# Optimization experiments

Measured on AMD Instinct MI355X. Metric: run time of the kernel, lower is better.

## Reference

```python
import jax, jax.numpy as jnp
import numpy as np
import math

N, S, C, K, V = 32, 4096, 1, 512, 128
TARGET_SCALE = 0.06  # normalize_scale == embedding_scale when normalize=True


def setup_inputs() -> dict:
    key = jax.random.key(0)
    k1, k2 = jax.random.split(key)
    x0 = jax.random.normal(k1, (N, S, C, V), dtype=jnp.float32)
    emb = jax.random.normal(k2, (C, K, V), dtype=jnp.float32) * TARGET_SCALE
    # after_update(): renormalize each code vector to norm = embedding_scale*sqrt(V)
    tn = TARGET_SCALE * math.sqrt(V)
    emb = emb * (tn / jnp.linalg.norm(emb, axis=2, keepdims=True))
    return {"x0": x0, "embedding0": emb}


def _vq_forward(x0, embedding0):
    tn = TARGET_SCALE * math.sqrt(V)
    # normalize inputs and codebook to the same norm (normalize=True path)
    x = tn * x0 / jnp.linalg.norm(x0, axis=3, keepdims=True)              # (N,S,C,V)
    emb = tn * embedding0 / jnp.linalg.norm(embedding0, axis=2, keepdims=True)  # (C,K,V)

    xf = x.reshape(N * S, C, V)
    x2 = jnp.sum(xf * xf, axis=2)                     # (NS, C)
    e2 = jnp.sum(emb * emb, axis=2)                   # (C, K)
    dots = jnp.einsum('ncv,ckv->nck', xf, emb)        # (NS, C, K)
    d2 = x2[:, :, None] + e2[None, :, :] - 2.0 * dots
    index = jnp.argmin(d2, axis=2)                    # (NS, C) int

    # entropy of code usage: histc over n_classes, normalized by len(index)=NS
    hist = jnp.zeros((K,), jnp.float32).at[index.reshape(-1)].add(1.0)
    prob = hist / float(N * S)
    entropy = -jnp.sum(jnp.where(hist > 0, prob * jnp.log(jnp.where(hist > 0, prob, 1.0)), 0.0))

    # gather selected code vectors per channel
    output = emb[jnp.arange(C)[None, :], index]       # (NS, C, V)
    output = output.reshape(x.shape)                  # (N,S,C,V)

    sg = jax.lax.stop_gradient
    out0 = sg(output - x) + x                                              # straight-through
    out1 = jnp.sum((sg(x) - output) ** 2, axis=3)                          # codebook loss (N,S,C)
    out2 = jnp.sum((x - sg(output)) ** 2, axis=3) + jnp.sum((x - x0) ** 2, axis=3)  # commitment + norm penalty
    return out0, out1, out2, entropy


def reference(x0, embedding0):
    return _vq_forward(x0, embedding0)
```

## Files before the change

### kernel.cpp

```cpp
#include <hip/hip_runtime.h>
#include <math.h>

#define VDIM   128
#define KCODES 512
#define NROWS  (32 * 4096)
#define TILE_ROWS 128
#define STAGE_CODES 128
#define STAGE_GRAN (STAGE_CODES * 16)
#define TN 0.67882250993908565f

typedef __attribute__((ext_vector_type(8))) short bf16x8;
typedef __attribute__((ext_vector_type(4))) float f32x4;

__device__ __forceinline__ unsigned short f2bf(float f) {
    unsigned u = __float_as_uint(f);
    unsigned r = u + 0x7FFFu + ((u >> 16) & 1u);
    return (unsigned short)(r >> 16);
}

__device__ __forceinline__ bf16x8 pack8(float4 a, float4 b) {
    bf16x8 v;
    v[0] = (short)f2bf(a.x); v[1] = (short)f2bf(a.y);
    v[2] = (short)f2bf(a.z); v[3] = (short)f2bf(a.w);
    v[4] = (short)f2bf(b.x); v[5] = (short)f2bf(b.y);
    v[6] = (short)f2bf(b.z); v[7] = (short)f2bf(b.w);
    return v;
}

__global__ void prep_emb(const float* __restrict__ emb0,
                         float* __restrict__ embn,
                         unsigned short* __restrict__ ebf) {
    int k = blockIdx.x;
    int l = threadIdx.x;
    const float* row = emb0 + (size_t)k * VDIM;
    float a = row[l];
    float b = row[l + 64];
    float ss = a * a + b * b;
    #pragma unroll
    for (int off = 32; off; off >>= 1) ss += __shfl_xor(ss, off);
    float nrm = sqrtf(ss);
    float ea = (TN * a) / nrm;
    float eb = (TN * b) / nrm;
    embn[(size_t)k * VDIM + l]      = ea;
    embn[(size_t)k * VDIM + l + 64] = eb;
    ebf[(size_t)k * VDIM + l]      = f2bf(ea);
    ebf[(size_t)k * VDIM + l + 64] = f2bf(eb);
}

__global__ __launch_bounds__(256, 4) void vq_main(
        const float* __restrict__ x0,
        const unsigned short* __restrict__ ebf,
        const float* __restrict__ embn,
        unsigned* __restrict__ hist,
        float* __restrict__ out0,
        float* __restrict__ out1,
        float* __restrict__ out2) {
    __shared__ uint4 sB[STAGE_GRAN];
    __shared__ int   sbesti[TILE_ROWS];
    __shared__ float sdot[TILE_ROWS];
    __shared__ float sn0[TILE_ROWS];

    int t = threadIdx.x;
    int w = t >> 6;
    int l = t & 63;
    int n15 = l & 15;
    int q = l >> 4;

    int rowbase = blockIdx.x * TILE_ROWS + (w << 5);
    bf16x8 afr[2][4];
    float nsq[2];
    #pragma unroll
    for (int s = 0; s < 2; ++s) {
        const float* xrow = x0 + (size_t)(rowbase + (s << 4) + n15) * VDIM + (q << 3);
        float p0 = 0.f, p1 = 0.f;
        #pragma unroll
        for (int kc = 0; kc < 4; ++kc) {
            const float4* xp = (const float4*)(xrow + (kc << 5));
            float4 a = xp[0], b = xp[1];
            p0 = fmaf(a.x, a.x, p0); p1 = fmaf(a.y, a.y, p1);
            p0 = fmaf(a.z, a.z, p0); p1 = fmaf(a.w, a.w, p1);
            p0 = fmaf(b.x, b.x, p0); p1 = fmaf(b.y, b.y, p1);
            p0 = fmaf(b.z, b.z, p0); p1 = fmaf(b.w, b.w, p1);
            afr[s][kc] = pack8(a, b);
        }
        nsq[s] = p0 + p1;
        nsq[s] += __shfl_xor(nsq[s], 16, 64);
        nsq[s] += __shfl_xor(nsq[s], 32, 64);
    }

    float best[2][4];
    int   bidx[2][4];
    #pragma unroll
    for (int s = 0; s < 2; ++s)
        #pragma unroll
        for (int r = 0; r < 4; ++r) { best[s][r] = -3.4e38f; bidx[s][r] = 0; }

    const f32x4 zero4 = {0.f, 0.f, 0.f, 0.f};
    const uint4* ebg = (const uint4*)ebf;

    for (int st = 0; st < 4; ++st) {
        if (st) __syncthreads();

        #pragma unroll
        for (int r = 0; r < 8; ++r) {
            int code = st * STAGE_CODES + (r << 4) + (t & 15);
            int gran = ((t >> 6) << 2) + ((t >> 4) & 3);
            sB[(r << 8) + t] = ebg[(size_t)code * 16 + gran];
        }
        __syncthreads();

        #pragma unroll 2
        for (int cn8 = 0; cn8 < 8; ++cn8) {
            const bf16x8* bls = ((const bf16x8*)sB) + (cn8 << 8) + l;
            bf16x8 b0 = bls[0], b1 = bls[64], b2 = bls[128], b3 = bls[192];
            int nbase = st * STAGE_CODES + (cn8 << 4) + n15;
            #pragma unroll
            for (int s = 0; s < 2; ++s) {
                f32x4 acc = __builtin_amdgcn_mfma_f32_16x16x32_bf16(afr[s][0], b0, zero4, 0, 0, 0);
                acc = __builtin_amdgcn_mfma_f32_16x16x32_bf16(afr[s][1], b1, acc, 0, 0, 0);
                acc = __builtin_amdgcn_mfma_f32_16x16x32_bf16(afr[s][2], b2, acc, 0, 0, 0);
                acc = __builtin_amdgcn_mfma_f32_16x16x32_bf16(afr[s][3], b3, acc, 0, 0, 0);
                #pragma unroll
                for (int r = 0; r < 4; ++r) {
                    float d = acc[r];
                    if (d > best[s][r]) { best[s][r] = d; bidx[s][r] = nbase; }
                }
            }
        }
    }

    #pragma unroll
    for (int m = 1; m <= 8; m <<= 1) {
        #pragma unroll
        for (int s = 0; s < 2; ++s)
            #pragma unroll
            for (int r = 0; r < 4; ++r) {
                float ov = __shfl_xor(best[s][r], m, 64);
                int   oi = __shfl_xor(bidx[s][r], m, 64);
                if (ov > best[s][r] || (ov == best[s][r] && oi < bidx[s][r])) {
                    best[s][r] = ov; bidx[s][r] = oi;
                }
            }
    }

    if (n15 == 0) {
        #pragma unroll
        for (int s = 0; s < 2; ++s)
            #pragma unroll
            for (int r = 0; r < 4; ++r) {
                int lr = (w << 5) + (s << 4) + (q << 2) + r;
                sbesti[lr] = bidx[s][r];
                sdot[lr]   = best[s][r];
            }
    }
    if (q == 0) {
        #pragma unroll
        for (int s = 0; s < 2; ++s) sn0[(w << 5) + (s << 4) + n15] = nsq[s];
    }
    __syncthreads();

    size_t blockrow = (size_t)blockIdx.x * TILE_ROWS;
    #pragma unroll
    for (int pass = 0; pass < 16; ++pass) {
        int lr = (pass << 3) + (t >> 5);
        int v4 = t & 31;
        int bi = sbesti[lr];
        float4 e = ((const float4*)(embn + (size_t)bi * VDIM))[v4];
        ((float4*)(out0 + (blockrow + lr) * (size_t)VDIM))[v4] = e;
    }

    if (t < TILE_ROWS) {
        size_t row = blockrow + t;
        int bi = sbesti[t];
        float dotv = sdot[t];
        float nn = sn0[t];
        float sc = TN / sqrtf(nn);
        float o1 = 2.f * TN * TN - 2.f * sc * dotv;
        out1[row] = o1;
        float sm = sc - 1.f;
        out2[row] = o1 + sm * sm * nn;
        atomicAdd(&hist[bi], 1u);
    }
}

__global__ void entropy_k(const unsigned* __restrict__ hist,
                          float* __restrict__ out) {
    __shared__ float red[8];
    int t = threadIdx.x;
    float h = (float)hist[t];
    float p = h / (float)NROWS;
    float term = (h > 0.f) ? p * logf(p) : 0.f;
    #pragma unroll
    for (int off = 32; off; off >>= 1) term += __shfl_xor(term, off);
    if ((t & 63) == 0) red[t >> 6] = term;
    __syncthreads();
    if (t == 0) {
        float ssum = 0.f;
        #pragma unroll
        for (int i = 0; i < 8; i++) ssum += red[i];
        out[0] = -ssum;
    }
}

extern "C" void kernel_launch(void* const* d_in, const int* in_sizes, int n_in,
                              void* d_out, int out_size, void* d_ws, size_t ws_size,
                              hipStream_t stream) {
    const float* x0   = (const float*)d_in[0];
    const float* emb0 = (const float*)d_in[1];

    float* embn = (float*)d_ws;
    unsigned* hist = (unsigned*)(embn + (size_t)KCODES * VDIM);
    unsigned short* ebf = (unsigned short*)(hist + KCODES);

    float* out  = (float*)d_out;
    float* out0 = out;
    float* out1 = out0 + (size_t)NROWS * VDIM;
    float* out2 = out1 + NROWS;
    float* oent = out2 + NROWS;

    hipMemsetAsync(hist, 0, KCODES * sizeof(unsigned), stream);
    prep_emb<<<KCODES, 64, 0, stream>>>(emb0, embn, ebf);
    vq_main<<<NROWS / TILE_ROWS, 256, 0, stream>>>(x0, ebf, embn, hist,
                                                   out0, out1, out2);
    entropy_k<<<1, KCODES, 0, stream>>>(hist, oent);
}
```

Before: 166.1 us.

## Halve row tile, fuse entropy into last block, gather output from bf16 codebook

Shrinks the row tile and code stage to 64, raising launch bounds to 8 waves so more blocks can be resident and hide memory latency. The entropy reduction moves into the main kernel using a last-block atomic counter, removing a separate launch. The fp32 normalized codebook buffer is dropped, and out0 is reconstructed from the bf16 codebook. This saves a buffer write, but the output now carries bf16 rounding error, and each block re-stages the full codebook for half as many rows.

```diff
diff --git a/kernel.cpp b/kernel.cpp
--- a/kernel.cpp
+++ b/kernel.cpp
@@ -4,8 +4,9 @@
 #define VDIM   128
 #define KCODES 512
 #define NROWS  (32 * 4096)
-#define TILE_ROWS 128
-#define STAGE_CODES 128
+#define TILE_ROWS 64
+#define NBLOCKS (NROWS / TILE_ROWS)
+#define STAGE_CODES 64
 #define STAGE_GRAN (STAGE_CODES * 16)
 #define TN 0.67882250993908565f
 
@@ -16,6 +17,10 @@
     unsigned u = __float_as_uint(f);
     unsigned r = u + 0x7FFFu + ((u >> 16) & 1u);
     return (unsigned short)(r >> 16);
+}
+
+__device__ __forceinline__ float bf2f(unsigned short h) {
+    return __uint_as_float(((unsigned)h) << 16);
 }
 
 __device__ __forceinline__ bf16x8 pack8(float4 a, float4 b) {
@@ -28,7 +33,6 @@
 }
 
 __global__ void prep_emb(const float* __restrict__ emb0,
-                         float* __restrict__ embn,
                          unsigned short* __restrict__ ebf) {
     int k = blockIdx.x;
     int l = threadIdx.x;
@@ -39,26 +43,25 @@
     #pragma unroll
     for (int off = 32; off; off >>= 1) ss += __shfl_xor(ss, off);
     float nrm = sqrtf(ss);
-    float ea = (TN * a) / nrm;
-    float eb = (TN * b) / nrm;
-    embn[(size_t)k * VDIM + l]      = ea;
-    embn[(size_t)k * VDIM + l + 64] = eb;
-    ebf[(size_t)k * VDIM + l]      = f2bf(ea);
-    ebf[(size_t)k * VDIM + l + 64] = f2bf(eb);
-}
-
-__global__ __launch_bounds__(256, 4) void vq_main(
+    ebf[(size_t)k * VDIM + l]      = f2bf((TN * a) / nrm);
+    ebf[(size_t)k * VDIM + l + 64] = f2bf((TN * b) / nrm);
+}
+
+__global__ __launch_bounds__(256, 8) void vq_main(
         const float* __restrict__ x0,
         const unsigned short* __restrict__ ebf,
-        const float* __restrict__ embn,
         unsigned* __restrict__ hist,
+        unsigned* __restrict__ counter,
         float* __restrict__ out0,
         float* __restrict__ out1,
-        float* __restrict__ out2) {
+        float* __restrict__ out2,
+        float* __restrict__ oent) {
     __shared__ uint4 sB[STAGE_GRAN];
     __shared__ int   sbesti[TILE_ROWS];
     __shared__ float sdot[TILE_ROWS];
     __shared__ float sn0[TILE_ROWS];
+    __shared__ float sred[8];
+    __shared__ int   slast;
 
     int t = threadIdx.x;
     int w = t >> 6;
@@ -66,12 +69,11 @@
     int n15 = l & 15;
     int q = l >> 4;
 
-    int rowbase = blockIdx.x * TILE_ROWS + (w << 5);
-    bf16x8 afr[2][4];
-    float nsq[2];
-    #pragma unroll
-    for (int s = 0; s < 2; ++s) {
-        const float* xrow = x0 + (size_t)(rowbase + (s << 4) + n15) * VDIM + (q << 3);
+    int rowbase = blockIdx.x * TILE_ROWS + (w << 4);
+    bf16x8 afr[4];
+    float nsq;
+    {
+        const float* xrow = x0 + (size_t)(rowbase + n15) * VDIM + (q << 3);
         float p0 = 0.f, p1 = 0.f;
         #pragma unroll
         for (int kc = 0; kc < 4; ++kc) {
@@ -81,91 +83,80 @@
             p0 = fmaf(a.z, a.z, p0); p1 = fmaf(a.w, a.w, p1);
             p0 = fmaf(b.x, b.x, p0); p1 = fmaf(b.y, b.y, p1);
             p0 = fmaf(b.z, b.z, p0); p1 = fmaf(b.w, b.w, p1);
-            afr[s][kc] = pack8(a, b);
-        }
-        nsq[s] = p0 + p1;
-        nsq[s] += __shfl_xor(nsq[s], 16, 64);
-        nsq[s] += __shfl_xor(nsq[s], 32, 64);
-    }
-
-    float best[2][4];
-    int   bidx[2][4];
-    #pragma unroll
-    for (int s = 0; s < 2; ++s)
-        #pragma unroll
-        for (int r = 0; r < 4; ++r) { best[s][r] = -3.4e38f; bidx[s][r] = 0; }
+            afr[kc] = pack8(a, b);
+        }
+        nsq = p0 + p1;
+        nsq += __shfl_xor(nsq, 16, 64);
+        nsq += __shfl_xor(nsq, 32, 64);
+    }
+
+    float best[4];
+    int   bidx[4];
+    #pragma unroll
+    for (int r = 0; r < 4; ++r) { best[r] = -3.4e38f; bidx[r] = 0; }
 
     const f32x4 zero4 = {0.f, 0.f, 0.f, 0.f};
     const uint4* ebg = (const uint4*)ebf;
 
-    for (int st = 0; st < 4; ++st) {
+    for (int st = 0; st < 8; ++st) {
         if (st) __syncthreads();
 
         #pragma unroll
-        for (int r = 0; r < 8; ++r) {
+        for (int r = 0; r < 4; ++r) {
             int code = st * STAGE_CODES + (r << 4) + (t & 15);
             int gran = ((t >> 6) << 2) + ((t >> 4) & 3);
             sB[(r << 8) + t] = ebg[(size_t)code * 16 + gran];
         }
         __syncthreads();
 
-        #pragma unroll 2
-        for (int cn8 = 0; cn8 < 8; ++cn8) {
-            const bf16x8* bls = ((const bf16x8*)sB) + (cn8 << 8) + l;
+        #pragma unroll
+        for (int c = 0; c < 4; ++c) {
+            const bf16x8* bls = ((const bf16x8*)sB) + (c << 8) + l;
             bf16x8 b0 = bls[0], b1 = bls[64], b2 = bls[128], b3 = bls[192];
-            int nbase = st * STAGE_CODES + (cn8 << 4) + n15;
-            #pragma unroll
-            for (int s = 0; s < 2; ++s) {
-                f32x4 acc = __builtin_amdgcn_mfma_f32_16x16x32_bf16(afr[s][0], b0, zero4, 0, 0, 0);
-                acc = __builtin_amdgcn_mfma_f32_16x16x32_bf16(afr[s][1], b1, acc, 0, 0, 0);
-                acc = __builtin_amdgcn_mfma_f32_16x16x32_bf16(afr[s][2], b2, acc, 0, 0, 0);
-                acc = __builtin_amdgcn_mfma_f32_16x16x32_bf16(afr[s][3], b3, acc, 0, 0, 0);
-                #pragma unroll
-                for (int r = 0; r < 4; ++r) {
-                    float d = acc[r];
-                    if (d > best[s][r]) { best[s][r] = d; bidx[s][r] = nbase; }
-                }
-            }
-        }
-    }
-
-    #pragma unroll
-    for (int m = 1; m <= 8; m <<= 1) {
-        #pragma unroll
-        for (int s = 0; s < 2; ++s)
+            int nbase = st * STAGE_CODES + (c << 4) + n15;
+            f32x4 acc = __builtin_amdgcn_mfma_f32_16x16x32_bf16(afr[0], b0, zero4, 0, 0, 0);
+            acc = __builtin_amdgcn_mfma_f32_16x16x32_bf16(afr[1], b1, acc, 0, 0, 0);
+            acc = __builtin_amdgcn_mfma_f32_16x16x32_bf16(afr[2], b2, acc, 0, 0, 0);
+            acc = __builtin_amdgcn_mfma_f32_16x16x32_bf16(afr[3], b3, acc, 0, 0, 0);
             #pragma unroll
             for (int r = 0; r < 4; ++r) {
-                float ov = __shfl_xor(best[s][r], m, 64);
-                int   oi = __shfl_xor(bidx[s][r], m, 64);
-                if (ov > best[s][r] || (ov == best[s][r] && oi < bidx[s][r])) {
-                    best[s][r] = ov; bidx[s][r] = oi;
-                }
+                float d = acc[r];
+                if (d > best[r]) { best[r] = d; bidx[r] = nbase; }
             }
+        }
+    }
+
+    #pragma unroll
+    for (int m = 1; m <= 8; m <<= 1) {
+        #pragma unroll
+        for (int r = 0; r < 4; ++r) {
+            float ov = __shfl_xor(best[r], m, 64);
+            int   oi = __shfl_xor(bidx[r], m, 64);
+            if (ov > best[r] || (ov == best[r] && oi < bidx[r])) {
+                best[r] = ov; bidx[r] = oi;
+            }
+        }
     }
 
     if (n15 == 0) {
         #pragma unroll
-        for (int s = 0; s < 2; ++s)
-            #pragma unroll
-            for (int r = 0; r < 4; ++r) {
-                int lr = (w << 5) + (s << 4) + (q << 2) + r;
-                sbesti[lr] = bidx[s][r];
-                sdot[lr]   = best[s][r];
-            }
-    }
-    if (q == 0) {
-        #pragma unroll
-        for (int s = 0; s < 2; ++s) sn0[(w << 5) + (s << 4) + n15] = nsq[s];
-    }
+        for (int r = 0; r < 4; ++r) {
+            int lr = (w << 4) + (q << 2) + r;
+            sbesti[lr] = bidx[r];
+            sdot[lr]   = best[r];
+        }
+    }
+    if (q == 0) sn0[(w << 4) + n15] = nsq;
     __syncthreads();
 
     size_t blockrow = (size_t)blockIdx.x * TILE_ROWS;
     #pragma unroll
-    for (int pass = 0; pass < 16; ++pass) {
+    for (int pass = 0; pass < 8; ++pass) {
         int lr = (pass << 3) + (t >> 5);
         int v4 = t & 31;
         int bi = sbesti[lr];
-        float4 e = ((const float4*)(embn + (size_t)bi * VDIM))[v4];
+        const unsigned short* ep = ebf + (size_t)bi * VDIM + (v4 << 2);
+        float4 e = make_float4(bf2f(ep[0]), bf2f(ep[1]), bf2f(ep[2]), bf2f(ep[3]));
         ((float4*)(out0 + (blockrow + lr) * (size_t)VDIM))[v4] = e;
     }
 
@@ -181,24 +172,35 @@
         out2[row] = o1 + sm * sm * nn;
         atomicAdd(&hist[bi], 1u);
     }
-}
-
-__global__ void entropy_k(const unsigned* __restrict__ hist,
-                          float* __restrict__ out) {
-    __shared__ float red[8];
-    int t = threadIdx.x;
-    float h = (float)hist[t];
-    float p = h / (float)NROWS;
-    float term = (h > 0.f) ? p * logf(p) : 0.f;
-    #pragma unroll
-    for (int off = 32; off; off >>= 1) term += __shfl_xor(term, off);
-    if ((t & 63) == 0) red[t >> 6] = term;
+
     __syncthreads();
     if (t == 0) {
-        float ssum = 0.f;
-        #pragma unroll
-        for (int i = 0; i < 8; i++) ssum += red[i];
-        out[0] = -ssum;
+        __threadfence();
+        unsigned prev = atomicAdd(counter, 1u);
+        slast = (prev == (unsigned)(NBLOCKS - 1));
+    }
+    __syncthreads();
+    if (slast) {
+        float term = 0.f;
+        #pragma unroll
+        for (int i = 0; i < 2; ++i) {
+            unsigned hv = __hip_atomic_load(&hist[t + (i << 8)],
+                                            __ATOMIC_RELAXED,
+                                            __HIP_MEMORY_SCOPE_AGENT);
+            float h = (float)hv;
+            if (h > 0.f) {
+                float p = h / (float)NROWS;
+                term += p * logf(p);
+            }
+        }
+        #pragma unroll
+        for (int off = 32; off; off >>= 1) term += __shfl_xor(term, off);
+        if (l == 0) sred[w] = term;
+        __syncthreads();
+        if (t == 0) {
+            float ssum = sred[0] + sred[1] + sred[2] + sred[3];
+            oent[0] = -ssum;
+        }
     }
 }
 
@@ -208,9 +210,9 @@
     const float* x0   = (const float*)d_in[0];
     const float* emb0 = (const float*)d_in[1];
 
-    float* embn = (float*)d_ws;
-    unsigned* hist = (unsigned*)(embn + (size_t)KCODES * VDIM);
-    unsigned short* ebf = (unsigned short*)(hist + KCODES);
+    unsigned short* ebf = (unsigned short*)d_ws;
+    unsigned* hist = (unsigned*)(ebf + (size_t)KCODES * VDIM);
+    unsigned* counter = hist + KCODES;
 
     float* out  = (float*)d_out;
     float* out0 = out;
@@ -218,9 +220,8 @@
     float* out2 = out1 + NROWS;
     float* oent = out2 + NROWS;
 
-    hipMemsetAsync(hist, 0, KCODES * sizeof(unsigned), stream);
-    prep_emb<<<KCODES, 64, 0, stream>>>(emb0, embn, ebf);
-    vq_main<<<NROWS / TILE_ROWS, 256, 0, stream>>>(x0, ebf, embn, hist,
-                                                   out0, out1, out2);
-    entropy_k<<<1, KCODES, 0, stream>>>(hist, oent);
-}
+    hipMemsetAsync(hist, 0, (KCODES + 1) * sizeof(unsigned), stream);
+    prep_emb<<<KCODES, 64, 0, stream>>>(emb0, ebf);
+    vq_main<<<NBLOCKS, 256, 0, stream>>>(x0, ebf, hist, counter,
+                                         out0, out1, out2, oent);
+}
```

New measurement: 215.4 us. 1.3x slower.
